# Performance work log

Hardware: AMD Instinct MI355X
Metric: run time of the kernel (lower is better)

The kernel has to match this reference:

```python
import jax, jax.numpy as jnp
import numpy as np

B, S = 8, 512                  # batch, seq_len
V, H, L = 30522, 768, 12       # vocab, hidden, layers
NH, F, T, P = 12, 3072, 2, 512 # heads, ffn dim, type vocab, max positions
D = H // NH
EPS = 1e-12


def layer_norm(x, scale, bias):
    mu = jnp.mean(x, axis=-1, keepdims=True)
    var = jnp.mean((x - mu) ** 2, axis=-1, keepdims=True)
    return (x - mu) * jax.lax.rsqrt(var + EPS) * scale + bias


def setup_inputs() -> dict:
    key = jax.random.key(0)
    ks = jax.random.split(key, 16)
    p = lambda k, shp: (0.02 * jax.random.normal(k, shp, dtype=jnp.float32))
    return {
        "input_ids": jax.random.randint(ks[0], (B, S), 0, V, dtype=jnp.int32),
        "type_ids": jax.random.randint(ks[1], (B, S), 0, T, dtype=jnp.int32),
        "word_emb": p(ks[2], (V, H)),
        "pos_emb": p(ks[3], (P, H)),
        "type_emb": p(ks[4], (T, H)),
        "emb_ln_scale": jnp.ones((H,), jnp.float32),
        "emb_ln_bias": jnp.zeros((H,), jnp.float32),
        "wq": p(ks[5], (L, H, H)), "bq": jnp.zeros((L, H), jnp.float32),
        "wk": p(ks[6], (L, H, H)), "bk": jnp.zeros((L, H), jnp.float32),
        "wv": p(ks[7], (L, H, H)), "bv": jnp.zeros((L, H), jnp.float32),
        "wo": p(ks[8], (L, H, H)), "bo": jnp.zeros((L, H), jnp.float32),
        "ln1_scale": jnp.ones((L, H), jnp.float32), "ln1_bias": jnp.zeros((L, H), jnp.float32),
        "w1": p(ks[9], (L, H, F)), "b1": jnp.zeros((L, F), jnp.float32),
        "w2": p(ks[10], (L, F, H)), "b2": jnp.zeros((L, H), jnp.float32),
        "ln2_scale": jnp.ones((L, H), jnp.float32), "ln2_bias": jnp.zeros((L, H), jnp.float32),
    }


def reference(input_ids, type_ids, word_emb, pos_emb, type_emb, emb_ln_scale,
              emb_ln_bias, wq, bq, wk, bk, wv, bv, wo, bo, ln1_scale, ln1_bias,
              w1, b1, w2, b2, ln2_scale, ln2_bias):
    # padding mask: 1.0 where token id == 0, shape [B,1,1,S]
    mask = (input_ids == 0).astype(jnp.float32)[:, None, None, :]
    # embeddings: word + position + segment, then layernorm (dropout off / eval)
    h = word_emb[input_ids] + pos_emb[None, :S, :] + type_emb[type_ids]
    h = layer_norm(h, emb_ln_scale, emb_ln_bias)

    def block(x, lp):
        (wq_, bq_, wk_, bk_, wv_, bv_, wo_, bo_, l1s, l1b,
         w1_, b1_, w2_, b2_, l2s, l2b) = lp
        def heads(y, w, b):  # [B,S,H] -> [B,NH,S,D]
            return (y @ w + b).reshape(B, S, NH, D).transpose(0, 2, 1, 3)
        q = heads(x, wq_, bq_)
        k = heads(x, wk_, bk_)
        v = heads(x, wv_, bv_)
        logits = jnp.einsum('bhqd,bhkd->bhqk', q, k) / jnp.sqrt(jnp.float32(D))
        logits = logits + mask * -10000.0
        attn = jax.nn.softmax(logits, axis=-1)
        ctx = jnp.einsum('bhqk,bhkd->bhqd', attn, v)
        ctx = ctx.transpose(0, 2, 1, 3).reshape(B, S, H)
        x = layer_norm(x + ctx @ wo_ + bo_, l1s, l1b)
        ffn = jax.nn.gelu(x @ w1_ + b1_, approximate=False) @ w2_ + b2_
        x = layer_norm(x + ffn, l2s, l2b)
        return x, None

    h, _ = jax.lax.scan(block, h, (wq, bq, wk, bk, wv, bv, wo, bo,
                                   ln1_scale, ln1_bias, w1, b1, w2, b2,
                                   ln2_scale, ln2_bias))
    return h
```

## Files before the change

### kernel.cpp

```cpp
#include <hip/hip_runtime.h>
#include <hip/hip_bf16.h>
#include <math.h>

#define S_LEN   512
#define HID     768
#define NLAYER  12
#define NHEAD   12
#define FFN_DIM 3072
#define HDIM    64
#define NTOK    4096
#define QKVN    2304

typedef __bf16 bf16x8 __attribute__((ext_vector_type(8)));
typedef __bf16 bf16x4 __attribute__((ext_vector_type(4)));
typedef float  f32x4  __attribute__((ext_vector_type(4)));

typedef __attribute__((address_space(1))) const unsigned int gas_u32;
typedef __attribute__((address_space(3))) unsigned int las_u32;

#define MFMA16(a, b, c) __builtin_amdgcn_mfma_f32_16x16x32_bf16((a), (b), (c), 0, 0, 0)

__device__ __forceinline__ float fast_gelu(float v) {
  float ax = fabsf(v) * 0.70710678118654752f;
  float t  = __builtin_amdgcn_rcpf(fmaf(0.3275911f, ax, 1.0f));
  float p  = fmaf(fmaf(fmaf(fmaf(1.061405429f, t, -1.453152027f), t,
                            1.421413741f), t, -0.284496736f), t, 0.254829592f);
  float e  = __expf(-ax * ax);
  float er = 1.0f - p * t * e;
  er = copysignf(er, v);
  return 0.5f * v * (1.0f + er);
}

__device__ __forceinline__ void block_reduce_2(float& sum, float& sq) {
  __shared__ float sd[8];
  int lane = threadIdx.x & 63;
  int wid  = threadIdx.x >> 6;
  #pragma unroll
  for (int off = 32; off > 0; off >>= 1) {
    sum += __shfl_down(sum, off, 64);
    sq  += __shfl_down(sq,  off, 64);
  }
  if (lane == 0) { sd[wid] = sum; sd[4 + wid] = sq; }
  __syncthreads();
  sum = sd[0] + sd[1] + sd[2] + sd[3];
  sq  = sd[4] + sd[5] + sd[6] + sd[7];
}

__global__ __launch_bounds__(256) void mask_kernel(const int* __restrict__ ids,
                                                   float* __restrict__ mb) {
  int i = blockIdx.x * 256 + threadIdx.x;
  if (i < NTOK) mb[i] = (ids[i] == 0) ? -10000.0f : 0.0f;
}

__global__ __launch_bounds__(256) void pack_qkvb_kernel(
    const float* __restrict__ bq, const float* __restrict__ bk,
    const float* __restrict__ bv, float* __restrict__ out) {
  int i = blockIdx.x * 256 + threadIdx.x;
  if (i >= NLAYER * QKVN) return;
  int l = i / QKVN, c = i % QKVN;
  float v = (c < HID) ? bq[l * HID + c]
          : (c < 2 * HID) ? bk[l * HID + c - HID]
                          : bv[l * HID + c - 2 * HID];
  out[i] = v;
}

__global__ __launch_bounds__(256) void embed_ln_kernel(
    const int* __restrict__ ids, const int* __restrict__ tids,
    const float* __restrict__ we, const float* __restrict__ pe,
    const float* __restrict__ te, const float* __restrict__ gamma,
    const float* __restrict__ beta, float* __restrict__ out32,
    __bf16* __restrict__ out16) {
  int t = blockIdx.x;
  int s = t & (S_LEN - 1);
  int id = ids[t];
  int tp = tids[t];
  float x[3];
  #pragma unroll
  for (int i = 0; i < 3; ++i) {
    int c = threadIdx.x + i * 256;
    x[i] = we[(size_t)id * HID + c] + pe[(size_t)s * HID + c] +
           te[(size_t)tp * HID + c];
  }
  float sum = x[0] + x[1] + x[2];
  float sq  = x[0]*x[0] + x[1]*x[1] + x[2]*x[2];
  block_reduce_2(sum, sq);
  float mu   = sum * (1.0f / HID);
  float var  = sq * (1.0f / HID) - mu * mu;
  float rstd = rsqrtf(var + 1e-12f);
  #pragma unroll
  for (int i = 0; i < 3; ++i) {
    int c = threadIdx.x + i * 256;
    float v = (x[i] - mu) * rstd * gamma[c] + beta[c];
    out32[(size_t)t * HID + c] = v;
    out16[(size_t)t * HID + c] = (__bf16)v;
  }
}

__global__ __launch_bounds__(256) void add_ln_kernel(
    const float* __restrict__ a, const float* __restrict__ b,
    const float* __restrict__ c,
    const float* __restrict__ gamma, const float* __restrict__ beta,
    float* __restrict__ out32, __bf16* __restrict__ out16) {
  int t = blockIdx.x;
  float x[3];
  #pragma unroll
  for (int i = 0; i < 3; ++i) {
    int ci = threadIdx.x + i * 256;
    size_t idx = (size_t)t * HID + ci;
    x[i] = a[idx] + b[idx];
    if (c) x[i] += c[idx];
  }
  float sum = x[0] + x[1] + x[2];
  float sq  = x[0]*x[0] + x[1]*x[1] + x[2]*x[2];
  block_reduce_2(sum, sq);
  float mu   = sum * (1.0f / HID);
  float var  = sq * (1.0f / HID) - mu * mu;
  float rstd = rsqrtf(var + 1e-12f);
  #pragma unroll
  for (int i = 0; i < 3; ++i) {
    int ci = threadIdx.x + i * 256;
    float v = (x[i] - mu) * rstd * gamma[ci] + beta[ci];
    out32[(size_t)t * HID + ci] = v;
    out16[(size_t)t * HID + ci] = (__bf16)v;
  }
}

__global__ __launch_bounds__(256) void tcvt_kernel(
    const float* __restrict__ src, __bf16* __restrict__ dst, int R, int C) {
  __shared__ float tile[32][33];
  int l = blockIdx.z;
  src += (size_t)l * R * C;
  dst += (size_t)l * R * C;
  int c0 = blockIdx.x * 32, r0 = blockIdx.y * 32;
  int tx = threadIdx.x & 31, ty = threadIdx.x >> 5;
  #pragma unroll
  for (int i = 0; i < 4; ++i) {
    int r = ty + i * 8;
    tile[r][tx] = src[(size_t)(r0 + r) * C + c0 + tx];
  }
  __syncthreads();
  #pragma unroll
  for (int i = 0; i < 4; ++i) {
    int r = ty + i * 8;
    dst[(size_t)(c0 + r) * R + r0 + tx] = (__bf16)tile[tx][r];
  }
}

__global__ __launch_bounds__(256) void tcvt4_kernel(
    const float* __restrict__ sq, const float* __restrict__ sk,
    const float* __restrict__ sv, const float* __restrict__ so,
    __bf16* __restrict__ dqkv, __bf16* __restrict__ dwo) {
  __shared__ float tile[32][33];
  const size_t WHH = (size_t)HID * HID;
  int z = blockIdx.z;
  int l = z >> 2, sel = z & 3;
  const float* src = ((sel == 0) ? sq : (sel == 1) ? sk : (sel == 2) ? sv : so)
                     + (size_t)l * WHH;
  __bf16* dst = (sel < 3) ? dqkv + (size_t)l * 3 * WHH + (size_t)sel * WHH
                          : dwo + (size_t)l * WHH;
  int c0 = blockIdx.x * 32, r0 = blockIdx.y * 32;
  int tx = threadIdx.x & 31, ty = threadIdx.x >> 5;
  #pragma unroll
  for (int i = 0; i < 4; ++i) {
    int r = ty + i * 8;
    tile[r][tx] = src[(size_t)(r0 + r) * HID + c0 + tx];
  }
  __syncthreads();
  #pragma unroll
  for (int i = 0; i < 4; ++i) {
    int r = ty + i * 8;
    dst[(size_t)(c0 + r) * HID + r0 + tx] = (__bf16)tile[tx][r];
  }
}

template <int MODE, int TN>
__global__ __launch_bounds__(256) void mfma_gemm(
    const __bf16* __restrict__ A, const __bf16* __restrict__ Bt,
    const float* __restrict__ bias, void* __restrict__ Cout,
    __bf16* __restrict__ vtout, int M, int N, int K, int kchunk) {
  constexpr int AI = 4;
  constexpr int BI = TN / 32;
  constexpr int RT = (TN == 128) ? 4 : 2;
  constexpr int CT = 4;
  __shared__ __align__(16) __bf16 As[128 * 64];
  __shared__ __align__(16) __bf16 Bs[TN * 64];
  const int tid = threadIdx.x;
  const int w = tid >> 6, lane = tid & 63;
  const int l15 = lane & 15, quad = lane >> 4;
  const int m0 = blockIdx.y * 128, n0 = blockIdx.x * TN;
  const int kz = blockIdx.z;
  const int lr = lane >> 3;
  const int colg = (lane & 7) ^ lr;

  const int wr = (TN == 128) ? (w >> 1) * 64 : w * 32;
  const int wc = (TN == 128) ? (w & 1) * 64 : 0;

  A  += (size_t)kz * kchunk;
  Bt += (size_t)kz * kchunk;

  f32x4 acc[RT][CT];
  const f32x4 z4 = {0.f, 0.f, 0.f, 0.f};
  #pragma unroll
  for (int i = 0; i < RT; ++i)
    #pragma unroll
    for (int j = 0; j < CT; ++j) acc[i][j] = z4;

  const __bf16* Ag = A  + (size_t)(m0 + 8 * AI * w + lr) * K + colg * 8;
  const __bf16* Bg = Bt + (size_t)(n0 + 8 * BI * w + lr) * K + colg * 8;
  __bf16* Al = As + 512 * AI * w;
  __bf16* Bl = Bs + 512 * BI * w;

  for (int kt = 0; kt < kchunk; kt += 64) {
    #pragma unroll
    for (int i = 0; i < AI; ++i)
      __builtin_amdgcn_global_load_lds(
          (gas_u32*)(Ag + (size_t)(8 * i) * K + kt),
          (las_u32*)(Al + 512 * i), 16, 0, 0);
    #pragma unroll
    for (int i = 0; i < BI; ++i)
      __builtin_amdgcn_global_load_lds(
          (gas_u32*)(Bg + (size_t)(8 * i) * K + kt),
          (las_u32*)(Bl + 512 * i), 16, 0, 0);
    __syncthreads();
    #pragma unroll
    for (int kc = 0; kc < 2; ++kc) {
      bf16x8 af[RT], bfr[CT];
      #pragma unroll
      for (int rt = 0; rt < RT; ++rt) {
        int row = wr + rt * 16 + l15;
        af[rt] = *(const bf16x8*)&As[(row * 8 + ((kc * 4 + quad) ^ (row & 7))) * 8];
      }
      #pragma unroll
      for (int ct = 0; ct < CT; ++ct) {
        int col = wc + ct * 16 + l15;
        bfr[ct] = *(const bf16x8*)&Bs[(col * 8 + ((kc * 4 + quad) ^ (col & 7))) * 8];
      }
      #pragma unroll
      for (int rt = 0; rt < RT; ++rt)
        #pragma unroll
        for (int ct = 0; ct < CT; ++ct)
          acc[rt][ct] = MFMA16(af[rt], bfr[ct], acc[rt][ct]);
    }
    __syncthreads();
  }

  float* outf = (float*)Cout + (size_t)kz * M * N;
  #pragma unroll
  for (int rt = 0; rt < RT; ++rt) {
    int rbase = m0 + wr + rt * 16 + quad * 4;
    #pragma unroll
    for (int ct = 0; ct < CT; ++ct) {
      int col = n0 + wc + ct * 16 + l15;
      float bv = (kz == 0) ? bias[col] : 0.0f;
      float vv[4];
      #pragma unroll
      for (int r = 0; r < 4; ++r) {
        float v = acc[rt][ct][r] + bv;
        if (MODE == 2) v = fast_gelu(v);
        vv[r] = v;
      }
      if (MODE == 3 && col >= 2 * HID) {
        int cc = col - 2 * HID;
        int hh = cc >> 6, d = cc & 63;
        int bb = rbase >> 9, s0 = rbase & (S_LEN - 1);
        bf16x4 pk = {(__bf16)vv[0], (__bf16)vv[1], (__bf16)vv[2], (__bf16)vv[3]};
        *(bf16x4*)(vtout +
                   (((size_t)(bb * NHEAD + hh) * HDIM + d) * S_LEN + s0)) = pk;
      } else {
        #pragma unroll
        for (int r = 0; r < 4; ++r) {
          if (MODE == 0)
            outf[(size_t)(rbase + r) * N + col] = vv[r];
          else
            ((__bf16*)Cout)[(size_t)(rbase + r) * N + col] = (__bf16)vv[r];
        }
      }
    }
  }
}

__global__ __launch_bounds__(256) void attn_mfma(
    const __bf16* __restrict__ qkv,
    const __bf16* __restrict__ vt,
    const float* __restrict__ mb,
    __bf16* __restrict__ ctx) {
  constexpr int PLD = 264;
  __shared__ __align__(16) __bf16 Plds[4][16 * PLD];
  const int tid = threadIdx.x;
  const int wv = tid >> 6, lane = tid & 63;
  const int l15 = lane & 15, quad = lane >> 4;
  const int b = blockIdx.z, hh = blockIdx.y, q0 = blockIdx.x * 64;
  const f32x4 z4 = {0.f, 0.f, 0.f, 0.f};

  size_t qoff = ((size_t)(b * S_LEN) + q0 + wv * 16 + l15) * QKVN + hh * HDIM;
  bf16x8 qa0 = *(const bf16x8*)(qkv + qoff + quad * 8);
  bf16x8 qa1 = *(const bf16x8*)(qkv + qoff + 32 + quad * 8);

  f32x4 sc[32];
  #pragma unroll
  for (int kt = 0; kt < 32; ++kt) {
    size_t koff = ((size_t)(b * S_LEN) + kt * 16 + l15) * QKVN + HID + hh * HDIM;
    bf16x8 kb0 = *(const bf16x8*)(qkv + koff + quad * 8);
    bf16x8 kb1 = *(const bf16x8*)(qkv + koff + 32 + quad * 8);
    f32x4 t = MFMA16(qa0, kb0, z4);
    sc[kt] = MFMA16(qa1, kb1, t);
  }

  float mx[4] = {-1e30f, -1e30f, -1e30f, -1e30f};
  #pragma unroll
  for (int kt = 0; kt < 32; ++kt) {
    float mval = mb[b * S_LEN + kt * 16 + l15];
    #pragma unroll
    for (int r = 0; r < 4; ++r) {
      float x = sc[kt][r] * 0.125f + mval;
      sc[kt][r] = x;
      mx[r] = fmaxf(mx[r], x);
    }
  }
  #pragma unroll
  for (int m = 1; m < 16; m <<= 1)
    #pragma unroll
    for (int r = 0; r < 4; ++r) mx[r] = fmaxf(mx[r], __shfl_xor(mx[r], m, 64));

  float sm[4] = {0.f, 0.f, 0.f, 0.f};
  #pragma unroll
  for (int kt = 0; kt < 32; ++kt)
    #pragma unroll
    for (int r = 0; r < 4; ++r) {
      float e = __expf(sc[kt][r] - mx[r]);
      sc[kt][r] = e;
      sm[r] += e;
    }
  #pragma unroll
  for (int m = 1; m < 16; m <<= 1)
    #pragma unroll
    for (int r = 0; r < 4; ++r) sm[r] += __shfl_xor(sm[r], m, 64);
  float inv[4];
  #pragma unroll
  for (int r = 0; r < 4; ++r) inv[r] = 1.0f / sm[r];

  __bf16* pbuf = &Plds[wv][0];
  const __bf16* vbase = vt + (size_t)(b * NHEAD + hh) * HDIM * S_LEN;
  f32x4 oc[4] = {z4, z4, z4, z4};
  #pragma unroll
  for (int half = 0; half < 2; ++half) {
    #pragma unroll
    for (int kt2 = 0; kt2 < 16; ++kt2) {
      int kt = half * 16 + kt2;
      #pragma unroll
      for (int r = 0; r < 4; ++r)
        pbuf[(quad * 4 + r) * PLD + kt2 * 16 + l15] = (__bf16)(sc[kt][r] * inv[r]);
    }
    #pragma unroll
    for (int kc = 0; kc < 8; ++kc) {
      bf16x8 pa = *(const bf16x8*)&pbuf[l15 * PLD + kc * 32 + quad * 8];
      int kbase = half * 256 + kc * 32;
      #pragma unroll
      for (int ct = 0; ct < 4; ++ct) {
        const __bf16* vp =
            vbase + (size_t)(ct * 16 + l15) * S_LEN + kbase + quad * 8;
        oc[ct] = MFMA16(pa, *(const bf16x8*)vp, oc[ct]);
      }
    }
  }

  int orow = b * S_LEN + q0 + wv * 16 + quad * 4;
  #pragma unroll
  for (int ct = 0; ct < 4; ++ct) {
    int col = hh * HDIM + ct * 16 + l15;
    #pragma unroll
    for (int r = 0; r < 4; ++r)
      ctx[(size_t)(orow + r) * HID + col] = (__bf16)oc[ct][r];
  }
}

extern "C" void kernel_launch(void* const* d_in, const int* in_sizes, int n_in,
                              void* d_out, int out_size, void* d_ws, size_t ws_size,
                              hipStream_t stream) {
  const int*   input_ids = (const int*)d_in[0];
  const int*   type_ids  = (const int*)d_in[1];
  const float* word_emb  = (const float*)d_in[2];
  const float* pos_emb   = (const float*)d_in[3];
  const float* type_emb  = (const float*)d_in[4];
  const float* eln_s     = (const float*)d_in[5];
  const float* eln_b     = (const float*)d_in[6];
  const float* wq = (const float*)d_in[7];
  const float* bq = (const float*)d_in[8];
  const float* wk = (const float*)d_in[9];
  const float* bk = (const float*)d_in[10];
  const float* wv = (const float*)d_in[11];
  const float* bv = (const float*)d_in[12];
  const float* wo = (const float*)d_in[13];
  const float* bo = (const float*)d_in[14];
  const float* l1s = (const float*)d_in[15];
  const float* l1b = (const float*)d_in[16];
  const float* w1  = (const float*)d_in[17];
  const float* b1  = (const float*)d_in[18];
  const float* w2  = (const float*)d_in[19];
  const float* b2  = (const float*)d_in[20];
  const float* l2s = (const float*)d_in[21];
  const float* l2b = (const float*)d_in[22];

  char* p = (char*)d_ws;
  float*   h32    = (float*)p;            p += (size_t)NTOK * HID * 4;
  float*   tmp32  = (float*)p;            p += (size_t)NTOK * HID * 4 * 2;
  float*   tmp32b = tmp32 + (size_t)NTOK * HID;
  __bf16*  vT16   = (__bf16*)tmp32;
  __bf16*  h16    = (__bf16*)p;           p += (size_t)NTOK * HID * 2;
  __bf16*  qkv16  = (__bf16*)p;           p += (size_t)NTOK * QKVN * 2;
  __bf16*  ctx16  = (__bf16*)p;           p += (size_t)NTOK * HID * 2;
  __bf16*  ffn16  = qkv16;
  float*   qkvb12 = (float*)p;            p += (size_t)NLAYER * QKVN * 4;
  float*   mb     = (float*)p;            p += (size_t)NTOK * 4;

  const size_t WHH = (size_t)HID * HID;
  const size_t WHF = (size_t)HID * FFN_DIM;
  const size_t WQKV = (size_t)QKVN * HID;

  size_t used = (size_t)(p - (char*)d_ws);
  size_t needB = used + (WQKV + WHH + 2 * WHF) * 2 * NLAYER + 256;
  int batched = (ws_size >= needB) ? 1 : 0;
  int nl = batched ? NLAYER : 1;
  __bf16* wTall  = (__bf16*)p;  p += WQKV * 2 * nl;
  __bf16* woTall = (__bf16*)p;  p += WHH * 2 * nl;
  __bf16* w1Tall = (__bf16*)p;  p += WHF * 2 * nl;
  __bf16* w2Tall = (__bf16*)p;  p += WHF * 2 * nl;
  size_t sQKV = batched ? WQKV : 0, sHH = batched ? WHH : 0,
         sHF = batched ? WHF : 0;

  dim3 blk(256);
  mask_kernel<<<dim3(NTOK / 256), blk, 0, stream>>>(input_ids, mb);
  pack_qkvb_kernel<<<dim3((NLAYER * QKVN + 255) / 256), blk, 0, stream>>>(
      bq, bk, bv, qkvb12);
  embed_ln_kernel<<<dim3(NTOK), blk, 0, stream>>>(
      input_ids, type_ids, word_emb, pos_emb, type_emb, eln_s, eln_b, h32, h16);

  if (batched) {
    tcvt4_kernel<<<dim3(HID / 32, HID / 32, 4 * NLAYER), blk, 0, stream>>>(
        wq, wk, wv, wo, wTall, woTall);
    tcvt_kernel<<<dim3(FFN_DIM / 32, HID / 32, NLAYER), blk, 0, stream>>>(
        w1, w1Tall, HID, FFN_DIM);
    tcvt_kernel<<<dim3(HID / 32, FFN_DIM / 32, NLAYER), blk, 0, stream>>>(
        w2, w2Tall, FFN_DIM, HID);
  }

  dim3 g_qkv(QKVN / 128, NTOK / 128, 1);
  dim3 g_ff1(FFN_DIM / 128, NTOK / 128, 1);
  dim3 g_wo(HID / 64, NTOK / 128, 1);
  dim3 g_ff2(HID / 64, NTOK / 128, 2);
  dim3 g_at(S_LEN / 64, NHEAD, 8);

  for (int l = 0; l < NLAYER; ++l) {
    size_t boff = (size_t)l * HID;
    if (!batched) {
      tcvt4_kernel<<<dim3(HID / 32, HID / 32, 4), blk, 0, stream>>>(
          wq + l * WHH, wk + l * WHH, wv + l * WHH, wo + l * WHH,
          wTall, woTall);
      tcvt_kernel<<<dim3(FFN_DIM / 32, HID / 32, 1), blk, 0, stream>>>(
          w1 + l * WHF, w1Tall, HID, FFN_DIM);
      tcvt_kernel<<<dim3(HID / 32, FFN_DIM / 32, 1), blk, 0, stream>>>(
          w2 + l * WHF, w2Tall, FFN_DIM, HID);
    }
    const __bf16* wTl  = wTall  + (size_t)l * sQKV;
    const __bf16* woTl = woTall + (size_t)l * sHH;
    const __bf16* w1Tl = w1Tall + (size_t)l * sHF;
    const __bf16* w2Tl = w2Tall + (size_t)l * sHF;

    mfma_gemm<3, 128><<<g_qkv, blk, 0, stream>>>(
        h16, wTl, qkvb12 + (size_t)l * QKVN, qkv16, vT16,
        NTOK, QKVN, HID, HID);
    attn_mfma<<<g_at, blk, 0, stream>>>(qkv16, vT16, mb, ctx16);
    mfma_gemm<0, 64><<<g_wo, blk, 0, stream>>>(
        ctx16, woTl, bo + boff, tmp32, nullptr, NTOK, HID, HID, HID);
    add_ln_kernel<<<dim3(NTOK), blk, 0, stream>>>(
        h32, tmp32, nullptr, l1s + boff, l1b + boff, h32, h16);
    mfma_gemm<2, 128><<<g_ff1, blk, 0, stream>>>(
        h16, w1Tl, b1 + (size_t)l * FFN_DIM, ffn16, nullptr,
        NTOK, FFN_DIM, HID, HID);
    mfma_gemm<0, 64><<<g_ff2, blk, 0, stream>>>(
        ffn16, w2Tl, b2 + boff, tmp32, nullptr, NTOK, HID, FFN_DIM,
        FFN_DIM / 2);
    float* dst = (l == NLAYER - 1) ? (float*)d_out : h32;
    add_ln_kernel<<<dim3(NTOK), blk, 0, stream>>>(
        h32, tmp32, tmp32b, l2s + boff, l2b + boff, dst, h16);
  }
}
```

Before: 2.699 ms.

## Add 256x256 eight-wave pipelined MFMA GEMM for QKV and FFN1 projections

Adds a new GEMM kernel with 256x256 output tiles, 512 threads, direct global-to-LDS loads, double-buffered LDS with explicit waitcnt/barrier ping-pong scheduling and setprio around MFMA bursts. The QKV and FFN1 projections use it in place of the 128-tile kernel. The aim is more data reuse per tile and overlap of loads with MFMA work. The trade-off is fewer blocks: 9x16 for QKV and 12x16 for FFN1, around 144-192 tiles on 256 CUs. That risks poor occupancy and wave quantization, and the large LDS footprint limits residency.

```diff
diff --git a/kernel.cpp b/kernel.cpp
--- a/kernel.cpp
+++ b/kernel.cpp
@@ -279,6 +279,155 @@
   }
 }
 
+#define BARX __builtin_amdgcn_s_barrier()
+#define LGKM0 do { asm volatile("s_waitcnt lgkmcnt(0)" ::: "memory"); \
+                   __builtin_amdgcn_sched_barrier(0); } while (0)
+#define VMCNT4 do { asm volatile("s_waitcnt vmcnt(4)" ::: "memory"); \
+                    __builtin_amdgcn_sched_barrier(0); } while (0)
+#define VMCNT0 do { asm volatile("s_waitcnt vmcnt(0)" ::: "memory"); \
+                    __builtin_amdgcn_sched_barrier(0); } while (0)
+#define PRIO1 __builtin_amdgcn_s_setprio(1)
+#define PRIO0 __builtin_amdgcn_s_setprio(0)
+
+#define G_LDS(src, dst) \
+  __builtin_amdgcn_global_load_lds((gas_u32*)(src), (las_u32*)(dst), 16, 0, 0)
+
+#define STAGE_A(bb, h, t) do {                                              \
+  G_LDS(Asrc + (size_t)((h)*128 + wv8) * Ksz + (size_t)(t)*64,              \
+        &As[bb][(h)*8192 + wv512]);                                         \
+  G_LDS(Asrc + (size_t)((h)*128 + 64 + wv8) * Ksz + (size_t)(t)*64,         \
+        &As[bb][(h)*8192 + 4096 + wv512]);                                  \
+} while (0)
+#define STAGE_B(bb, h, t) do {                                              \
+  G_LDS(Bsrc + (size_t)((h)*128 + wv8) * Ksz + (size_t)(t)*64,              \
+        &Bs[bb][(h)*8192 + wv512]);                                         \
+  G_LDS(Bsrc + (size_t)((h)*128 + 64 + wv8) * Ksz + (size_t)(t)*64,         \
+        &Bs[bb][(h)*8192 + 4096 + wv512]);                                  \
+} while (0)
+
+#define RD_A(bb, fmo, dst) do {                                             \
+  _Pragma("unroll") for (int f = 0; f < 4; ++f) {                           \
+    dst[f][0] = *(const bf16x8*)&As[bb][aoff + ((fmo) + f) * 1024 + xr0];   \
+    dst[f][1] = *(const bf16x8*)&As[bb][aoff + ((fmo) + f) * 1024 + xr1];   \
+  } } while (0)
+#define RD_B(bb, fno, dst) do {                                             \
+  _Pragma("unroll") for (int f = 0; f < 2; ++f) {                           \
+    dst[f][0] = *(const bf16x8*)&Bs[bb][boff + ((fno) + f) * 1024 + xr0];   \
+    dst[f][1] = *(const bf16x8*)&Bs[bb][boff + ((fno) + f) * 1024 + xr1];   \
+  } } while (0)
+
+#define MMQ(am, bn, mo, no) do {                                            \
+  _Pragma("unroll") for (int f = 0; f < 4; ++f)                             \
+  _Pragma("unroll") for (int g = 0; g < 2; ++g) {                           \
+    acc[(mo) + f][(no) + g] = MFMA16(am[f][0], bn[g][0], acc[(mo)+f][(no)+g]); \
+    acc[(mo) + f][(no) + g] = MFMA16(am[f][1], bn[g][1], acc[(mo)+f][(no)+g]); \
+  } } while (0)
+
+template <int MODE>
+__global__ __launch_bounds__(512, 2) void mfma_gemm256(
+    const __bf16* __restrict__ A, const __bf16* __restrict__ Bt,
+    const float* __restrict__ bias, void* __restrict__ Cout,
+    __bf16* __restrict__ vtout, int M, int N, int K) {
+  __shared__ __align__(16) __bf16 As[2][256 * 64];
+  __shared__ __align__(16) __bf16 Bs[2][256 * 64];
+  const int tid = threadIdx.x;
+  const int w = tid >> 6, lane = tid & 63;
+  const int l15 = lane & 15, quad = lane >> 4;
+  const int wm = w >> 2, wn = w & 3;
+  const int m0 = blockIdx.y * 256, n0 = blockIdx.x * 256;
+  const int lr = lane >> 3;
+  const int colg = ((lane & 7) ^ lr) * 8;
+  const int wv8 = w * 8, wv512 = w * 512;
+  const size_t Ksz = K;
+
+  const int aoff = wm * 8192 + l15 * 64;
+  const int boff = (wn >> 1) * 8192 + (wn & 1) * 4096 + l15 * 64;
+  const int xr0 = (quad ^ (l15 & 7)) * 8;
+  const int xr1 = xr0 ^ 32;
+
+  const __bf16* Asrc = A  + (size_t)(m0 + lr) * Ksz + colg;
+  const __bf16* Bsrc = Bt + (size_t)(n0 + lr) * Ksz + colg;
+
+  f32x4 acc[8][4];
+  const f32x4 z4 = {0.f, 0.f, 0.f, 0.f};
+  #pragma unroll
+  for (int i = 0; i < 8; ++i)
+    #pragma unroll
+    for (int j = 0; j < 4; ++j) acc[i][j] = z4;
+
+  const int NT = K >> 6;
+  const int NI = NT >> 1;
+
+  STAGE_B(0, 0, 0); STAGE_B(0, 1, 0);
+  STAGE_A(0, 0, 0); STAGE_A(0, 1, 0);
+  STAGE_B(1, 0, 1); STAGE_B(1, 1, 1);
+  VMCNT4;
+  BARX;
+
+  bf16x8 aL[4][2], aH[4][2], bL[2][2], bH[2][2];
+
+  for (int i = 0; i < NI; ++i) {
+    const int T1 = 2 * i + 1, T2 = 2 * i + 2, T3 = 2 * i + 3;
+    const bool s2 = (T2 < NT), s3 = (T3 < NT), last = (i == NI - 1);
+
+    RD_A(0, 0, aL); RD_B(0, 0, bL);
+    STAGE_A(1, 0, T1);
+    BARX; LGKM0; PRIO1; MMQ(aL, bL, 0, 0); PRIO0; BARX;
+    RD_B(0, 2, bH);
+    STAGE_A(1, 1, T1);
+    BARX; LGKM0; PRIO1; MMQ(aL, bH, 0, 2); PRIO0; BARX;
+    RD_A(0, 4, aH);
+    if (s2) STAGE_B(0, 0, T2);
+    BARX; LGKM0; PRIO1; MMQ(aH, bH, 4, 2); PRIO0; BARX;
+    if (s2) STAGE_B(0, 1, T2);
+    BARX; PRIO1; MMQ(aH, bL, 4, 0); PRIO0;
+    if (last) { VMCNT0; } else { VMCNT4; }
+    BARX;
+    RD_A(1, 0, aL); RD_B(1, 0, bL);
+    if (s2) STAGE_A(0, 0, T2);
+    BARX; LGKM0; PRIO1; MMQ(aL, bL, 0, 0); PRIO0; BARX;
+    RD_B(1, 2, bH);
+    if (s2) STAGE_A(0, 1, T2);
+    BARX; LGKM0; PRIO1; MMQ(aL, bH, 0, 2); PRIO0; BARX;
+    RD_A(1, 4, aH);
+    if (s3) STAGE_B(1, 0, T3);
+    BARX; LGKM0; PRIO1; MMQ(aH, bH, 4, 2); PRIO0; BARX;
+    if (s3) STAGE_B(1, 1, T3);
+    BARX; PRIO1; MMQ(aH, bL, 4, 0); PRIO0;
+    if (!last) { VMCNT4; }
+    BARX;
+  }
+
+  #pragma unroll
+  for (int fm = 0; fm < 8; ++fm) {
+    int rbase = m0 + wm * 128 + fm * 16 + quad * 4;
+    #pragma unroll
+    for (int fn = 0; fn < 4; ++fn) {
+      int col = n0 + wn * 64 + fn * 16 + l15;
+      float bv = bias[col];
+      float vv[4];
+      #pragma unroll
+      for (int r = 0; r < 4; ++r) {
+        float v = acc[fm][fn][r] + bv;
+        if (MODE == 2) v = fast_gelu(v);
+        vv[r] = v;
+      }
+      if (MODE == 3 && col >= 2 * HID) {
+        int cc = col - 2 * HID;
+        int hh = cc >> 6, d = cc & 63;
+        int bb = rbase >> 9, s0 = rbase & (S_LEN - 1);
+        bf16x4 pk = {(__bf16)vv[0], (__bf16)vv[1], (__bf16)vv[2], (__bf16)vv[3]};
+        *(bf16x4*)(vtout +
+                   (((size_t)(bb * NHEAD + hh) * HDIM + d) * S_LEN + s0)) = pk;
+      } else {
+        #pragma unroll
+        for (int r = 0; r < 4; ++r)
+          ((__bf16*)Cout)[(size_t)(rbase + r) * N + col] = (__bf16)vv[r];
+      }
+    }
+  }
+}
+
 __global__ __launch_bounds__(256) void attn_mfma(
     const __bf16* __restrict__ qkv,
     const __bf16* __restrict__ vt,
@@ -428,7 +577,7 @@
   size_t sQKV = batched ? WQKV : 0, sHH = batched ? WHH : 0,
          sHF = batched ? WHF : 0;
 
-  dim3 blk(256);
+  dim3 blk(256), blk512(512);
   mask_kernel<<<dim3(NTOK / 256), blk, 0, stream>>>(input_ids, mb);
   pack_qkvb_kernel<<<dim3((NLAYER * QKVN + 255) / 256), blk, 0, stream>>>(
       bq, bk, bv, qkvb12);
@@ -444,8 +593,8 @@
         w2, w2Tall, FFN_DIM, HID);
   }
 
-  dim3 g_qkv(QKVN / 128, NTOK / 128, 1);
-  dim3 g_ff1(FFN_DIM / 128, NTOK / 128, 1);
+  dim3 g_qkv(QKVN / 256, NTOK / 256, 1);
+  dim3 g_ff1(FFN_DIM / 256, NTOK / 256, 1);
   dim3 g_wo(HID / 64, NTOK / 128, 1);
   dim3 g_ff2(HID / 64, NTOK / 128, 2);
   dim3 g_at(S_LEN / 64, NHEAD, 8);
@@ -466,17 +615,17 @@
     const __bf16* w1Tl = w1Tall + (size_t)l * sHF;
     const __bf16* w2Tl = w2Tall + (size_t)l * sHF;
 
-    mfma_gemm<3, 128><<<g_qkv, blk, 0, stream>>>(
+    mfma_gemm256<3><<<g_qkv, blk512, 0, stream>>>(
         h16, wTl, qkvb12 + (size_t)l * QKVN, qkv16, vT16,
-        NTOK, QKVN, HID, HID);
+        NTOK, QKVN, HID);
     attn_mfma<<<g_at, blk, 0, stream>>>(qkv16, vT16, mb, ctx16);
     mfma_gemm<0, 64><<<g_wo, blk, 0, stream>>>(
         ctx16, woTl, bo + boff, tmp32, nullptr, NTOK, HID, HID, HID);
     add_ln_kernel<<<dim3(NTOK), blk, 0, stream>>>(
         h32, tmp32, nullptr, l1s + boff, l1b + boff, h32, h16);
-    mfma_gemm<2, 128><<<g_ff1, blk, 0, stream>>>(
+    mfma_gemm256<2><<<g_ff1, blk512, 0, stream>>>(
         h16, w1Tl, b1 + (size_t)l * FFN_DIM, ffn16, nullptr,
-        NTOK, FFN_DIM, HID, HID);
+        NTOK, FFN_DIM, HID);
     mfma_gemm<0, 64><<<g_ff2, blk, 0, stream>>>(
         ffn16, w2Tl, b2 + boff, tmp32, nullptr, NTOK, HID, FFN_DIM,
         FFN_DIM / 2);
```

Measured after the change: 2.844 ms. 5.4% more time.
